# Performance work log

Measured on AMD Instinct MI355X. Metric: run time of the kernel, lower is better.

## Reference

```python
import jax, jax.numpy as jnp
import numpy as np

DIM = 1024
HEADS = 16
DIM_HEAD = 64
INNER = HEADS * DIM_HEAD
SCALE = 8.0  # default scale in plain_cosine_sim_attention
EPS = 1e-5


def setup_inputs() -> dict:
    key = jax.random.key(0)
    ks = jax.random.split(key, 5)
    b, n = 2, 2048
    x = jax.random.normal(ks[0], (b, n, DIM), dtype=jnp.float32)
    ln_w = jnp.ones((DIM,), dtype=jnp.float32)
    ln_b = jnp.zeros((DIM,), dtype=jnp.float32)
    W_qkv = jax.random.normal(ks[1], (DIM, 3 * INNER), dtype=jnp.float32) * (DIM ** -0.5)
    W_out = jax.random.normal(ks[2], (INNER, DIM), dtype=jnp.float32) * (INNER ** -0.5)
    return {"x": x, "ln_w": ln_w, "ln_b": ln_b, "W_qkv": W_qkv, "W_out": W_out}


def _l2norm(t):
    return t / jnp.clip(jnp.linalg.norm(t, axis=-1, keepdims=True), 1e-12)


def reference(x, ln_w, ln_b, W_qkv, W_out):
    b, n, _ = x.shape
    # LayerNorm
    mu = jnp.mean(x, axis=-1, keepdims=True)
    var = jnp.var(x, axis=-1, keepdims=True)
    xn = (x - mu) * jax.lax.rsqrt(var + EPS) * ln_w + ln_b
    # QKV projection (no bias)
    qkv = xn @ W_qkv  # [b, n, 3*inner]
    q, k, v = jnp.split(qkv, 3, axis=-1)
    # [b, n, h*d] -> [b, h, n, d]
    def to_heads(t):
        return t.reshape(b, n, HEADS, DIM_HEAD).transpose(0, 2, 1, 3)
    q, k, v = to_heads(q), to_heads(k), to_heads(v)
    # cosine-sim attention: l2-normalize q, k then scaled dot product
    q = _l2norm(q)
    k = _l2norm(k)
    sim = jnp.einsum('bhid,bhjd->bhij', q, k) * SCALE
    # causal mask
    causal = jnp.tril(jnp.ones((n, n), dtype=bool))
    sim = jnp.where(causal, sim, jnp.finfo(sim.dtype).min)
    attn = jax.nn.softmax(sim, axis=-1)
    o = jnp.einsum('bhij,bhjd->bhid', attn, v)
    # [b, h, n, d] -> [b, n, h*d]
    o = o.transpose(0, 2, 1, 3).reshape(b, n, INNER)
    return o @ W_out
```

## Files before the change

kernel.cpp:

```cpp
#include <hip/hip_runtime.h>
#include <hip/hip_bf16.h>

typedef __attribute__((ext_vector_type(8))) short short8;
typedef __attribute__((ext_vector_type(4))) float floatx4;

__device__ __forceinline__ ushort f2bf(float f) {
    union { __hip_bfloat16 h; ushort u; } cv;
    cv.h = __float2bfloat16(f);
    return cv.u;
}
__device__ __forceinline__ float bf2f(ushort u) {
    union { ushort u; __hip_bfloat16 h; } cv;
    cv.u = u;
    return __bfloat162float(cv.h);
}
__device__ __forceinline__ ushort f2bf_rtz(float f) {
    union { float f; unsigned u; } cv;
    cv.f = f;
    return (ushort)(cv.u >> 16);
}

typedef __attribute__((address_space(1))) void* gas1_t;
typedef __attribute__((address_space(3))) void* las3_t;
__device__ __forceinline__ void cp16(const ushort* g, ushort* l) {
    __builtin_amdgcn_global_load_lds((gas1_t)(unsigned long long)g,
                                     (las3_t)(unsigned long long)l, 16, 0, 0);
}

__global__ __launch_bounds__(256) void transpose_cast2(const float* __restrict__ Wqkv,
                                                       const float* __restrict__ Wout,
                                                       ushort* __restrict__ WqkvT,
                                                       ushort* __restrict__ WoutT) {
    __shared__ float tile[32][33];
    int bx = blockIdx.x, by = blockIdx.y;
    const float* in; ushort* out; int R = 1024, C;
    if (bx < 96) { in = Wqkv; out = WqkvT; C = 3072; }
    else { in = Wout; out = WoutT; C = 1024; bx -= 96; }
    int c0 = bx * 32, r0 = by * 32;
    int tx = threadIdx.x, ty = threadIdx.y;
    for (int j = 0; j < 32; j += 8)
        tile[ty + j][tx] = in[(size_t)(r0 + ty + j) * C + c0 + tx];
    __syncthreads();
    for (int j = 0; j < 32; j += 8)
        out[(size_t)(c0 + ty + j) * R + r0 + tx] = f2bf(tile[tx][ty + j]);
}

__global__ __launch_bounds__(256) void ln_kernel(const float* __restrict__ x,
                                                 const float* __restrict__ lw,
                                                 const float* __restrict__ lb,
                                                 ushort* __restrict__ xn) {
    int row = blockIdx.x;
    int tid = threadIdx.x;
    const float4* xr = (const float4*)(x + (size_t)row * 1024);
    float4 v = xr[tid];
    float s = v.x + v.y + v.z + v.w;
    float sq = v.x * v.x + v.y * v.y + v.z * v.z + v.w * v.w;
    for (int off = 32; off; off >>= 1) {
        s += __shfl_xor(s, off);
        sq += __shfl_xor(sq, off);
    }
    __shared__ float ls[4], lq[4];
    int wave = tid >> 6, lane = tid & 63;
    if (lane == 0) { ls[wave] = s; lq[wave] = sq; }
    __syncthreads();
    s = ls[0] + ls[1] + ls[2] + ls[3];
    sq = lq[0] + lq[1] + lq[2] + lq[3];
    float mu = s * (1.0f / 1024.0f);
    float var = sq * (1.0f / 1024.0f) - mu * mu;
    float rs = rsqrtf(var + 1e-5f);
    const float4* wr = (const float4*)lw;
    const float4* br = (const float4*)lb;
    float4 wv = wr[tid], bv = br[tid];
    ushort4 o;
    o.x = f2bf((v.x - mu) * rs * wv.x + bv.x);
    o.y = f2bf((v.y - mu) * rs * wv.y + bv.y);
    o.z = f2bf((v.z - mu) * rs * wv.z + bv.z);
    o.w = f2bf((v.w - mu) * rs * wv.w + bv.w);
    *(ushort4*)&xn[(size_t)row * 1024 + tid * 4] = o;
}

__global__ __launch_bounds__(256) void gemm_qkv_fused(const ushort* __restrict__ A,
                                                      const ushort* __restrict__ Bt,
                                                      ushort* __restrict__ Qt,
                                                      ushort* __restrict__ Kt,
                                                      ushort* __restrict__ Vb) {
    __shared__ ushort smem[18432];
    const int K = 1024, T = 32;
    const int tid = threadIdx.x;
    const int wave = tid >> 6, lane = tid & 63;
    const int quad = lane >> 4, l15 = lane & 15;
    const int wm = (wave >> 1) * 64, wn = (wave & 1) * 64;
    const int bm = blockIdx.y * 128, bn = blockIdx.x;

    const int s0 = tid, s1 = tid + 256;
    const int row0 = s0 >> 2, src0 = (s0 & 3) ^ (row0 & 3);
    const int row1 = s1 >> 2, src1 = (s1 & 3) ^ (row1 & 3);

    floatx4 acc[4][4];
    floatx4 z4 = {0.f, 0.f, 0.f, 0.f};
    for (int mi = 0; mi < 4; mi++)
        for (int ni = 0; ni < 4; ni++) acc[mi][ni] = z4;

    const ushort* Ap0 = A + (size_t)(bm + row0) * K + src0 * 8;
    const ushort* Ap1 = A + (size_t)(bm + row1) * K + src1 * 8;
    const ushort* Bp0 = Bt + (size_t)(bn * 128 + row0) * K + src0 * 8;
    const ushort* Bp1 = Bt + (size_t)(bn * 128 + row1) * K + src1 * 8;

    ushort* As = smem;
    ushort* Bs = smem + 8192;

    cp16(Ap0, &As[wave * 512]);
    cp16(Ap1, &As[2048 + wave * 512]);
    cp16(Bp0, &Bs[wave * 512]);
    cp16(Bp1, &Bs[2048 + wave * 512]);

    for (int t = 0; t < T; t++) {
        __syncthreads();
        if (t + 1 < T) {
            const int nb = (t + 1) & 1;
            const int k0n = (t + 1) << 5;
            cp16(Ap0 + k0n, &As[nb * 4096 + wave * 512]);
            cp16(Ap1 + k0n, &As[nb * 4096 + 2048 + wave * 512]);
            cp16(Bp0 + k0n, &Bs[nb * 4096 + wave * 512]);
            cp16(Bp1 + k0n, &Bs[nb * 4096 + 2048 + wave * 512]);
        }
        const ushort* Ab = As + (t & 1) * 4096;
        const ushort* Bb = Bs + (t & 1) * 4096;
        short8 af[4], bfr[4];
        for (int mi = 0; mi < 4; mi++) {
            int ra = wm + mi * 16 + l15;
            af[mi] = *(const short8*)&Ab[ra * 32 + ((quad ^ (ra & 3)) << 3)];
        }
        for (int ni = 0; ni < 4; ni++) {
            int rb = wn + ni * 16 + l15;
            bfr[ni] = *(const short8*)&Bb[rb * 32 + ((quad ^ (rb & 3)) << 3)];
        }
        for (int mi = 0; mi < 4; mi++)
            for (int ni = 0; ni < 4; ni++)
                acc[mi][ni] = __builtin_amdgcn_mfma_f32_16x16x32_bf16(
                    af[mi], bfr[ni], acc[mi][ni], 0, 0, 0);
    }

    const int col_base = bn * 128 + wn;
    const int type = col_base >> 10;
    const int h = (col_base & 1023) >> 6;
    const int row_base = bm + wm;

    if (type < 2) {
        ushort* dst = (type == 0) ? Qt : Kt;
        for (int mi = 0; mi < 4; mi++) {
            for (int r = 0; r < 4; r++) {
                float ss = 0.f;
                for (int ni = 0; ni < 4; ni++) ss += acc[mi][ni][r] * acc[mi][ni][r];
                for (int off = 1; off < 16; off <<= 1) ss += __shfl_xor(ss, off);
                float inv = rsqrtf(fmaxf(ss, 1e-24f));
                int rg = row_base + mi * 16 + quad * 4 + r;
                int bb = rg >> 11, n = rg & 2047;
                size_t orow = ((size_t)(bb * 16 + h) * 2048 + n) * 64;
                for (int ni = 0; ni < 4; ni++)
                    dst[orow + ni * 16 + l15] = f2bf(acc[mi][ni][r] * inv);
            }
        }
    } else {
        __syncthreads();
        ushort* tr = smem + wave * 4608;
        for (int mi = 0; mi < 4; mi++)
            for (int ni = 0; ni < 4; ni++)
                for (int r = 0; r < 4; r++) {
                    int row_l = mi * 16 + quad * 4 + r;
                    int col_l = ni * 16 + l15;
                    tr[col_l * 72 + row_l] = f2bf(acc[mi][ni][r]);
                }
        int bb = row_base >> 11, n0 = row_base & 2047;
        size_t vbase = ((size_t)(bb * 16 + h) * 32 + (n0 >> 6)) * 4096;
        const int dl = lane >> 3, nc = (lane & 7) * 8;
        for (int i = 0; i < 8; i++) {
            int d = dl + i * 8;
            short8 val = *(const short8*)&tr[d * 72 + nc];
            *(short8*)&Vb[vbase + (size_t)d * 64 + nc] = val;
        }
    }
}

__global__ __launch_bounds__(256) void gemm_out(const ushort* __restrict__ A,
                                                const ushort* __restrict__ Bt,
                                                float* __restrict__ C,
                                                int M, int N, int K) {
    __shared__ ushort As[2][128 * 32];
    __shared__ ushort Bs[2][128 * 32];
    const int tid = threadIdx.x;
    const int wave = tid >> 6, lane = tid & 63;
    const int quad = lane >> 4, l15 = lane & 15;
    const int wm = (wave >> 1) * 64, wn = (wave & 1) * 64;
    const int bm = blockIdx.y * 128, bn = blockIdx.x * 128;

    const int s0 = tid, s1 = tid + 256;
    const int row0 = s0 >> 2, src0 = (s0 & 3) ^ (row0 & 3);
    const int row1 = s1 >> 2, src1 = (s1 & 3) ^ (row1 & 3);

    floatx4 acc[4][4];
    floatx4 z4 = {0.f, 0.f, 0.f, 0.f};
    for (int mi = 0; mi < 4; mi++)
        for (int ni = 0; ni < 4; ni++) acc[mi][ni] = z4;

    const ushort* Ap0 = A + (size_t)(bm + row0) * K + src0 * 8;
    const ushort* Ap1 = A + (size_t)(bm + row1) * K + src1 * 8;
    const ushort* Bp0 = Bt + (size_t)(bn + row0) * K + src0 * 8;
    const ushort* Bp1 = Bt + (size_t)(bn + row1) * K + src1 * 8;

    const int T = K >> 5;
    cp16(Ap0, &As[0][wave * 512]);
    cp16(Ap1, &As[0][2048 + wave * 512]);
    cp16(Bp0, &Bs[0][wave * 512]);
    cp16(Bp1, &Bs[0][2048 + wave * 512]);

    for (int t = 0; t < T; t++) {
        __syncthreads();
        if (t + 1 < T) {
            const int nb = (t + 1) & 1;
            const int k0n = (t + 1) << 5;
            cp16(Ap0 + k0n, &As[nb][wave * 512]);
            cp16(Ap1 + k0n, &As[nb][2048 + wave * 512]);
            cp16(Bp0 + k0n, &Bs[nb][wave * 512]);
            cp16(Bp1 + k0n, &Bs[nb][2048 + wave * 512]);
        }
        const ushort* Ab = As[t & 1];
        const ushort* Bb = Bs[t & 1];
        short8 af[4], bfr[4];
        for (int mi = 0; mi < 4; mi++) {
            int ra = wm + mi * 16 + l15;
            af[mi] = *(const short8*)&Ab[ra * 32 + ((quad ^ (ra & 3)) << 3)];
        }
        for (int ni = 0; ni < 4; ni++) {
            int rb = wn + ni * 16 + l15;
            bfr[ni] = *(const short8*)&Bb[rb * 32 + ((quad ^ (rb & 3)) << 3)];
        }
        for (int mi = 0; mi < 4; mi++)
            for (int ni = 0; ni < 4; ni++)
                acc[mi][ni] = __builtin_amdgcn_mfma_f32_16x16x32_bf16(
                    af[mi], bfr[ni], acc[mi][ni], 0, 0, 0);
    }
    for (int mi = 0; mi < 4; mi++)
        for (int ni = 0; ni < 4; ni++)
            for (int r = 0; r < 4; r++) {
                int row = bm + wm + mi * 16 + quad * 4 + r;
                int col = bn + wn + ni * 16 + l15;
                C[(size_t)row * N + col] = acc[mi][ni][r];
            }
}

#define LOG2E8 11.541560327111707f

__global__ __launch_bounds__(256) void flash_attn(const ushort* __restrict__ Qt,
                                                  const ushort* __restrict__ Kt,
                                                  const ushort* __restrict__ Vb,
                                                  ushort* __restrict__ O) {
    const int id = blockIdx.x;
    const int xcd = id & 7, r_ = id >> 3;
    const int bh = xcd * 4 + (r_ >> 5);
    const int qt = r_ & 31;
    const int b = bh >> 4, h = bh & 15;
    const int q0 = qt * 64;
    const int tid = threadIdx.x;
    const int wave = tid >> 6, lane = tid & 63;
    const int quad = lane >> 4, l15 = lane & 15;

    __shared__ ushort Ks[2][64 * 64];
    __shared__ ushort Vs[2][64 * 64];
    __shared__ ushort Ps[4][16 * 64];

    const int ch0 = tid, ch1 = tid + 256;
    const int r0 = ch0 >> 3, sg0 = (ch0 & 7) ^ (r0 & 7);
    const int r1 = ch1 >> 3, sg1 = (ch1 & 7) ^ (r1 & 7);

    const ushort* Kp0 = Kt + ((size_t)bh * 2048 + r0) * 64 + sg0 * 8;
    const ushort* Kp1 = Kt + ((size_t)bh * 2048 + r1) * 64 + sg1 * 8;
    const ushort* Vp0 = Vb + (size_t)bh * 131072 + r0 * 64 + sg0 * 8;
    const ushort* Vp1 = Vb + (size_t)bh * 131072 + r1 * 64 + sg1 * 8;

    floatx4 z4 = {0.f, 0.f, 0.f, 0.f};

    const ushort* Qp = Qt + ((size_t)bh * 2048 + q0 + wave * 16 + l15) * 64;
    short8 qf0 = *(const short8*)(Qp + quad * 8);
    short8 qf1 = *(const short8*)(Qp + 32 + quad * 8);

    float rs_acc[4] = {0.f, 0.f, 0.f, 0.f};
    floatx4 o_acc[4];
    for (int ni = 0; ni < 4; ni++) o_acc[ni] = z4;

    cp16(Kp0, &Ks[0][wave * 512]);
    cp16(Kp1, &Ks[0][2048 + wave * 512]);
    cp16(Vp0, &Vs[0][wave * 512]);
    cp16(Vp1, &Vs[0][2048 + wave * 512]);

    for (int kt = 0; kt <= qt; kt++) {
        __syncthreads();
        if (kt < qt) {
            const int nb2 = (kt + 1) & 1;
            const size_t to = (size_t)(kt + 1) * 4096;
            cp16(Kp0 + to, &Ks[nb2][wave * 512]);
            cp16(Kp1 + to, &Ks[nb2][2048 + wave * 512]);
            cp16(Vp0 + to, &Vs[nb2][wave * 512]);
            cp16(Vp1 + to, &Vs[nb2][2048 + wave * 512]);
        }
        const ushort* Kb = Ks[kt & 1];
        const ushort* Vb_ = Vs[kt & 1];

        floatx4 s_acc[4];
        for (int ni = 0; ni < 4; ni++) s_acc[ni] = z4;
        for (int ni = 0; ni < 4; ni++) {
            int rb = ni * 16 + l15;
            short8 kf0 = *(const short8*)&Kb[rb * 64 + ((quad ^ (rb & 7)) << 3)];
            short8 kf1 = *(const short8*)&Kb[rb * 64 + (((quad + 4) ^ (rb & 7)) << 3)];
            s_acc[ni] = __builtin_amdgcn_mfma_f32_16x16x32_bf16(qf0, kf0, s_acc[ni], 0, 0, 0);
            s_acc[ni] = __builtin_amdgcn_mfma_f32_16x16x32_bf16(qf1, kf1, s_acc[ni], 0, 0, 0);
        }

        const bool diag = (kt == qt);
        for (int ni = 0; ni < 4; ni++) {
            const int col_loc = ni * 16 + l15;
            const int chnk = col_loc >> 3;
            for (int r = 0; r < 4; r++) {
                const int row_l = quad * 4 + r;
                float e = __builtin_amdgcn_exp2f(
                    fmaf(s_acc[ni][r], LOG2E8, -LOG2E8));
                if (diag && col_loc > wave * 16 + row_l) e = 0.f;
                rs_acc[r] += e;
                Ps[wave][row_l * 64 + (((chnk ^ (row_l & 7)) << 3) | (col_loc & 7))] =
                    f2bf_rtz(e);
            }
        }

        short8 pa0 = *(const short8*)&Ps[wave][l15 * 64 + ((quad ^ (l15 & 7)) << 3)];
        short8 pa1 = *(const short8*)&Ps[wave][l15 * 64 + (((quad + 4) ^ (l15 & 7)) << 3)];
        for (int ni = 0; ni < 4; ni++) {
            int rv = ni * 16 + l15;
            short8 v0 = *(const short8*)&Vb_[rv * 64 + ((quad ^ (rv & 7)) << 3)];
            short8 v1 = *(const short8*)&Vb_[rv * 64 + (((quad + 4) ^ (rv & 7)) << 3)];
            o_acc[ni] = __builtin_amdgcn_mfma_f32_16x16x32_bf16(pa0, v0, o_acc[ni], 0, 0, 0);
            o_acc[ni] = __builtin_amdgcn_mfma_f32_16x16x32_bf16(pa1, v1, o_acc[ni], 0, 0, 0);
        }
    }

    for (int r = 0; r < 4; r++) {
        float rs = rs_acc[r];
        for (int off = 1; off < 16; off <<= 1) rs += __shfl_xor(rs, off);
        float inv = 1.0f / rs;
        int grow = q0 + wave * 16 + quad * 4 + r;
        size_t rowbase = ((size_t)b * 2048 + grow) * 1024 + h * 64;
        for (int ni = 0; ni < 4; ni++)
            O[rowbase + ni * 16 + l15] = f2bf(o_acc[ni][r] * inv);
    }
}

extern "C" void kernel_launch(void* const* d_in, const int* in_sizes, int n_in,
                              void* d_out, int out_size, void* d_ws, size_t ws_size,
                              hipStream_t stream) {
    const float* x = (const float*)d_in[0];
    const float* ln_w = (const float*)d_in[1];
    const float* ln_b = (const float*)d_in[2];
    const float* W_qkv = (const float*)d_in[3];
    const float* W_out = (const float*)d_in[4];

    char* w = (char*)d_ws;
    ushort* xn    = (ushort*)(w);
    ushort* WqkvT = (ushort*)(w + (8ull << 20));
    ushort* WoutT = (ushort*)(w + (14ull << 20));
    ushort* Vb    = (ushort*)(w + (16ull << 20));
    ushort* Qt    = (ushort*)(w + (24ull << 20));
    ushort* Kt    = (ushort*)(w + (32ull << 20));
    ushort* obuf  = (ushort*)(w + (40ull << 20));

    transpose_cast2<<<dim3(128, 32), dim3(32, 8), 0, stream>>>(W_qkv, W_out, WqkvT, WoutT);
    ln_kernel<<<4096, 256, 0, stream>>>(x, ln_w, ln_b, xn);
    gemm_qkv_fused<<<dim3(24, 32), 256, 0, stream>>>(xn, WqkvT, Qt, Kt, Vb);
    flash_attn<<<1024, 256, 0, stream>>>(Qt, Kt, Vb, obuf);
    gemm_out<<<dim3(8, 32), 256, 0, stream>>>(obuf, WoutT, (float*)d_out, 4096, 1024, 1024);
}
```

Before: 191.2 us.

## Merge weight prep with layernorm, swizzle QKV GEMM grid, pair causal attention tiles

Three separate changes. The weight transpose/cast and layernorm now run as one launch, which removes a kernel boundary. The QKV GEMM grid becomes 1D with an XCD-aware remap, so blocks sharing A rows land on the same XCD for L2 reuse. Flash attention now has each block handle a pair of query tiles (i and 31-i), which balances causal work across blocks at the cost of halving the block count to 512 and serializing two passes.

Result: faster. 181.0 us (-5.3%).

```diff
diff --git a/kernel.cpp b/kernel.cpp
--- a/kernel.cpp
+++ b/kernel.cpp
@@ -27,56 +27,58 @@
                                      (las3_t)(unsigned long long)l, 16, 0, 0);
 }
 
-__global__ __launch_bounds__(256) void transpose_cast2(const float* __restrict__ Wqkv,
-                                                       const float* __restrict__ Wout,
-                                                       ushort* __restrict__ WqkvT,
-                                                       ushort* __restrict__ WoutT) {
-    __shared__ float tile[32][33];
-    int bx = blockIdx.x, by = blockIdx.y;
-    const float* in; ushort* out; int R = 1024, C;
-    if (bx < 96) { in = Wqkv; out = WqkvT; C = 3072; }
-    else { in = Wout; out = WoutT; C = 1024; bx -= 96; }
-    int c0 = bx * 32, r0 = by * 32;
-    int tx = threadIdx.x, ty = threadIdx.y;
-    for (int j = 0; j < 32; j += 8)
-        tile[ty + j][tx] = in[(size_t)(r0 + ty + j) * C + c0 + tx];
-    __syncthreads();
-    for (int j = 0; j < 32; j += 8)
-        out[(size_t)(c0 + ty + j) * R + r0 + tx] = f2bf(tile[tx][ty + j]);
-}
-
-__global__ __launch_bounds__(256) void ln_kernel(const float* __restrict__ x,
+__global__ __launch_bounds__(256) void prep_w_ln(const float* __restrict__ Wqkv,
+                                                 const float* __restrict__ Wout,
+                                                 ushort* __restrict__ WqkvT,
+                                                 ushort* __restrict__ WoutT,
+                                                 const float* __restrict__ x,
                                                  const float* __restrict__ lw,
                                                  const float* __restrict__ lb,
                                                  ushort* __restrict__ xn) {
-    int row = blockIdx.x;
-    int tid = threadIdx.x;
-    const float4* xr = (const float4*)(x + (size_t)row * 1024);
-    float4 v = xr[tid];
-    float s = v.x + v.y + v.z + v.w;
-    float sq = v.x * v.x + v.y * v.y + v.z * v.z + v.w * v.w;
-    for (int off = 32; off; off >>= 1) {
-        s += __shfl_xor(s, off);
-        sq += __shfl_xor(sq, off);
-    }
-    __shared__ float ls[4], lq[4];
-    int wave = tid >> 6, lane = tid & 63;
-    if (lane == 0) { ls[wave] = s; lq[wave] = sq; }
-    __syncthreads();
-    s = ls[0] + ls[1] + ls[2] + ls[3];
-    sq = lq[0] + lq[1] + lq[2] + lq[3];
-    float mu = s * (1.0f / 1024.0f);
-    float var = sq * (1.0f / 1024.0f) - mu * mu;
-    float rs = rsqrtf(var + 1e-5f);
-    const float4* wr = (const float4*)lw;
-    const float4* br = (const float4*)lb;
-    float4 wv = wr[tid], bv = br[tid];
-    ushort4 o;
-    o.x = f2bf((v.x - mu) * rs * wv.x + bv.x);
-    o.y = f2bf((v.y - mu) * rs * wv.y + bv.y);
-    o.z = f2bf((v.z - mu) * rs * wv.z + bv.z);
-    o.w = f2bf((v.w - mu) * rs * wv.w + bv.w);
-    *(ushort4*)&xn[(size_t)row * 1024 + tid * 4] = o;
+    const int id = blockIdx.x;
+    const int tid = threadIdx.x;
+    if (id < 4096) {
+        __shared__ float tile[32][33];
+        int bx = id & 127, by = id >> 7;
+        const float* in; ushort* out; int R = 1024, C;
+        if (bx < 96) { in = Wqkv; out = WqkvT; C = 3072; }
+        else { in = Wout; out = WoutT; C = 1024; bx -= 96; }
+        int c0 = bx * 32, r0 = by * 32;
+        int tx = tid & 31, ty = tid >> 5;
+        for (int j = 0; j < 32; j += 8)
+            tile[ty + j][tx] = in[(size_t)(r0 + ty + j) * C + c0 + tx];
+        __syncthreads();
+        for (int j = 0; j < 32; j += 8)
+            out[(size_t)(c0 + ty + j) * R + r0 + tx] = f2bf(tile[tx][ty + j]);
+    } else {
+        int row = id - 4096;
+        const float4* xr = (const float4*)(x + (size_t)row * 1024);
+        float4 v = xr[tid];
+        float s = v.x + v.y + v.z + v.w;
+        float sq = v.x * v.x + v.y * v.y + v.z * v.z + v.w * v.w;
+        for (int off = 32; off; off >>= 1) {
+            s += __shfl_xor(s, off);
+            sq += __shfl_xor(sq, off);
+        }
+        __shared__ float ls[4], lq[4];
+        int wave = tid >> 6, lane = tid & 63;
+        if (lane == 0) { ls[wave] = s; lq[wave] = sq; }
+        __syncthreads();
+        s = ls[0] + ls[1] + ls[2] + ls[3];
+        sq = lq[0] + lq[1] + lq[2] + lq[3];
+        float mu = s * (1.0f / 1024.0f);
+        float var = sq * (1.0f / 1024.0f) - mu * mu;
+        float rs = rsqrtf(var + 1e-5f);
+        const float4* wr = (const float4*)lw;
+        const float4* br = (const float4*)lb;
+        float4 wv = wr[tid], bv = br[tid];
+        ushort4 o;
+        o.x = f2bf((v.x - mu) * rs * wv.x + bv.x);
+        o.y = f2bf((v.y - mu) * rs * wv.y + bv.y);
+        o.z = f2bf((v.z - mu) * rs * wv.z + bv.z);
+        o.w = f2bf((v.w - mu) * rs * wv.w + bv.w);
+        *(ushort4*)&xn[(size_t)row * 1024 + tid * 4] = o;
+    }
 }
 
 __global__ __launch_bounds__(256) void gemm_qkv_fused(const ushort* __restrict__ A,
@@ -86,11 +88,14 @@
                                                       ushort* __restrict__ Vb) {
     __shared__ ushort smem[18432];
     const int K = 1024, T = 32;
+    const int id = blockIdx.x;
+    const int xcd = id & 7, r_ = id >> 3;
+    const int bm = (xcd * 4 + r_ / 24) * 128;
+    const int bn = r_ % 24;
     const int tid = threadIdx.x;
     const int wave = tid >> 6, lane = tid & 63;
     const int quad = lane >> 4, l15 = lane & 15;
     const int wm = (wave >> 1) * 64, wn = (wave & 1) * 64;
-    const int bm = blockIdx.y * 128, bn = blockIdx.x;
 
     const int s0 = tid, s1 = tid + 256;
     const int row0 = s0 >> 2, src0 = (s0 & 3) ^ (row0 & 3);
@@ -257,10 +262,9 @@
                                                   ushort* __restrict__ O) {
     const int id = blockIdx.x;
     const int xcd = id & 7, r_ = id >> 3;
-    const int bh = xcd * 4 + (r_ >> 5);
-    const int qt = r_ & 31;
+    const int bh = xcd * 4 + (r_ >> 4);
+    const int pairi = r_ & 15;
     const int b = bh >> 4, h = bh & 15;
-    const int q0 = qt * 64;
     const int tid = threadIdx.x;
     const int wave = tid >> 6, lane = tid & 63;
     const int quad = lane >> 4, l15 = lane & 15;
@@ -280,76 +284,82 @@
 
     floatx4 z4 = {0.f, 0.f, 0.f, 0.f};
 
-    const ushort* Qp = Qt + ((size_t)bh * 2048 + q0 + wave * 16 + l15) * 64;
-    short8 qf0 = *(const short8*)(Qp + quad * 8);
-    short8 qf1 = *(const short8*)(Qp + 32 + quad * 8);
-
-    float rs_acc[4] = {0.f, 0.f, 0.f, 0.f};
-    floatx4 o_acc[4];
-    for (int ni = 0; ni < 4; ni++) o_acc[ni] = z4;
-
-    cp16(Kp0, &Ks[0][wave * 512]);
-    cp16(Kp1, &Ks[0][2048 + wave * 512]);
-    cp16(Vp0, &Vs[0][wave * 512]);
-    cp16(Vp1, &Vs[0][2048 + wave * 512]);
-
-    for (int kt = 0; kt <= qt; kt++) {
-        __syncthreads();
-        if (kt < qt) {
-            const int nb2 = (kt + 1) & 1;
-            const size_t to = (size_t)(kt + 1) * 4096;
-            cp16(Kp0 + to, &Ks[nb2][wave * 512]);
-            cp16(Kp1 + to, &Ks[nb2][2048 + wave * 512]);
-            cp16(Vp0 + to, &Vs[nb2][wave * 512]);
-            cp16(Vp1 + to, &Vs[nb2][2048 + wave * 512]);
-        }
-        const ushort* Kb = Ks[kt & 1];
-        const ushort* Vb_ = Vs[kt & 1];
-
-        floatx4 s_acc[4];
-        for (int ni = 0; ni < 4; ni++) s_acc[ni] = z4;
-        for (int ni = 0; ni < 4; ni++) {
-            int rb = ni * 16 + l15;
-            short8 kf0 = *(const short8*)&Kb[rb * 64 + ((quad ^ (rb & 7)) << 3)];
-            short8 kf1 = *(const short8*)&Kb[rb * 64 + (((quad + 4) ^ (rb & 7)) << 3)];
-            s_acc[ni] = __builtin_amdgcn_mfma_f32_16x16x32_bf16(qf0, kf0, s_acc[ni], 0, 0, 0);
-            s_acc[ni] = __builtin_amdgcn_mfma_f32_16x16x32_bf16(qf1, kf1, s_acc[ni], 0, 0, 0);
-        }
-
-        const bool diag = (kt == qt);
-        for (int ni = 0; ni < 4; ni++) {
-            const int col_loc = ni * 16 + l15;
-            const int chnk = col_loc >> 3;
-            for (int r = 0; r < 4; r++) {
-                const int row_l = quad * 4 + r;
-                float e = __builtin_amdgcn_exp2f(
-                    fmaf(s_acc[ni][r], LOG2E8, -LOG2E8));
-                if (diag && col_loc > wave * 16 + row_l) e = 0.f;
-                rs_acc[r] += e;
-                Ps[wave][row_l * 64 + (((chnk ^ (row_l & 7)) << 3) | (col_loc & 7))] =
-                    f2bf_rtz(e);
-            }
-        }
-
-        short8 pa0 = *(const short8*)&Ps[wave][l15 * 64 + ((quad ^ (l15 & 7)) << 3)];
-        short8 pa1 = *(const short8*)&Ps[wave][l15 * 64 + (((quad + 4) ^ (l15 & 7)) << 3)];
-        for (int ni = 0; ni < 4; ni++) {
-            int rv = ni * 16 + l15;
-            short8 v0 = *(const short8*)&Vb_[rv * 64 + ((quad ^ (rv & 7)) << 3)];
-            short8 v1 = *(const short8*)&Vb_[rv * 64 + (((quad + 4) ^ (rv & 7)) << 3)];
-            o_acc[ni] = __builtin_amdgcn_mfma_f32_16x16x32_bf16(pa0, v0, o_acc[ni], 0, 0, 0);
-            o_acc[ni] = __builtin_amdgcn_mfma_f32_16x16x32_bf16(pa1, v1, o_acc[ni], 0, 0, 0);
-        }
-    }
-
-    for (int r = 0; r < 4; r++) {
-        float rs = rs_acc[r];
-        for (int off = 1; off < 16; off <<= 1) rs += __shfl_xor(rs, off);
-        float inv = 1.0f / rs;
-        int grow = q0 + wave * 16 + quad * 4 + r;
-        size_t rowbase = ((size_t)b * 2048 + grow) * 1024 + h * 64;
-        for (int ni = 0; ni < 4; ni++)
-            O[rowbase + ni * 16 + l15] = f2bf(o_acc[ni][r] * inv);
+    for (int pass = 0; pass < 2; pass++) {
+        const int qt = pass ? (31 - pairi) : pairi;
+        const int q0 = qt * 64;
+
+        const ushort* Qp = Qt + ((size_t)bh * 2048 + q0 + wave * 16 + l15) * 64;
+        short8 qf0 = *(const short8*)(Qp + quad * 8);
+        short8 qf1 = *(const short8*)(Qp + 32 + quad * 8);
+
+        float rs_acc[4] = {0.f, 0.f, 0.f, 0.f};
+        floatx4 o_acc[4];
+        for (int ni = 0; ni < 4; ni++) o_acc[ni] = z4;
+
+        __syncthreads();
+        cp16(Kp0, &Ks[0][wave * 512]);
+        cp16(Kp1, &Ks[0][2048 + wave * 512]);
+        cp16(Vp0, &Vs[0][wave * 512]);
+        cp16(Vp1, &Vs[0][2048 + wave * 512]);
+
+        for (int kt = 0; kt <= qt; kt++) {
+            __syncthreads();
+            if (kt < qt) {
+                const int nb2 = (kt + 1) & 1;
+                const size_t to = (size_t)(kt + 1) * 4096;
+                cp16(Kp0 + to, &Ks[nb2][wave * 512]);
+                cp16(Kp1 + to, &Ks[nb2][2048 + wave * 512]);
+                cp16(Vp0 + to, &Vs[nb2][wave * 512]);
+                cp16(Vp1 + to, &Vs[nb2][2048 + wave * 512]);
+            }
+            const ushort* Kb = Ks[kt & 1];
+            const ushort* Vb_ = Vs[kt & 1];
+
+            floatx4 s_acc[4];
+            for (int ni = 0; ni < 4; ni++) s_acc[ni] = z4;
+            for (int ni = 0; ni < 4; ni++) {
+                int rb = ni * 16 + l15;
+                short8 kf0 = *(const short8*)&Kb[rb * 64 + ((quad ^ (rb & 7)) << 3)];
+                short8 kf1 = *(const short8*)&Kb[rb * 64 + (((quad + 4) ^ (rb & 7)) << 3)];
+                s_acc[ni] = __builtin_amdgcn_mfma_f32_16x16x32_bf16(qf0, kf0, s_acc[ni], 0, 0, 0);
+                s_acc[ni] = __builtin_amdgcn_mfma_f32_16x16x32_bf16(qf1, kf1, s_acc[ni], 0, 0, 0);
+            }
+
+            const bool diag = (kt == qt);
+            for (int ni = 0; ni < 4; ni++) {
+                const int col_loc = ni * 16 + l15;
+                const int chnk = col_loc >> 3;
+                for (int r = 0; r < 4; r++) {
+                    const int row_l = quad * 4 + r;
+                    float e = __builtin_amdgcn_exp2f(
+                        fmaf(s_acc[ni][r], LOG2E8, -LOG2E8));
+                    if (diag && col_loc > wave * 16 + row_l) e = 0.f;
+                    rs_acc[r] += e;
+                    Ps[wave][row_l * 64 + (((chnk ^ (row_l & 7)) << 3) | (col_loc & 7))] =
+                        f2bf_rtz(e);
+                }
+            }
+
+            short8 pa0 = *(const short8*)&Ps[wave][l15 * 64 + ((quad ^ (l15 & 7)) << 3)];
+            short8 pa1 = *(const short8*)&Ps[wave][l15 * 64 + (((quad + 4) ^ (l15 & 7)) << 3)];
+            for (int ni = 0; ni < 4; ni++) {
+                int rv = ni * 16 + l15;
+                short8 v0 = *(const short8*)&Vb_[rv * 64 + ((quad ^ (rv & 7)) << 3)];
+                short8 v1 = *(const short8*)&Vb_[rv * 64 + (((quad + 4) ^ (rv & 7)) << 3)];
+                o_acc[ni] = __builtin_amdgcn_mfma_f32_16x16x32_bf16(pa0, v0, o_acc[ni], 0, 0, 0);
+                o_acc[ni] = __builtin_amdgcn_mfma_f32_16x16x32_bf16(pa1, v1, o_acc[ni], 0, 0, 0);
+            }
+        }
+
+        for (int r = 0; r < 4; r++) {
+            float rs = rs_acc[r];
+            for (int off = 1; off < 16; off <<= 1) rs += __shfl_xor(rs, off);
+            float inv = 1.0f / rs;
+            int grow = q0 + wave * 16 + quad * 4 + r;
+            size_t rowbase = ((size_t)b * 2048 + grow) * 1024 + h * 64;
+            for (int ni = 0; ni < 4; ni++)
+                O[rowbase + ni * 16 + l15] = f2bf(o_acc[ni][r] * inv);
+        }
     }
 }
 
@@ -371,9 +381,8 @@
     ushort* Kt    = (ushort*)(w + (32ull << 20));
     ushort* obuf  = (ushort*)(w + (40ull << 20));
 
-    transpose_cast2<<<dim3(128, 32), dim3(32, 8), 0, stream>>>(W_qkv, W_out, WqkvT, WoutT);
-    ln_kernel<<<4096, 256, 0, stream>>>(x, ln_w, ln_b, xn);
-    gemm_qkv_fused<<<dim3(24, 32), 256, 0, stream>>>(xn, WqkvT, Qt, Kt, Vb);
-    flash_attn<<<1024, 256, 0, stream>>>(Qt, Kt, Vb, obuf);
+    prep_w_ln<<<8192, 256, 0, stream>>>(W_qkv, W_out, WqkvT, WoutT, x, ln_w, ln_b, xn);
+    gemm_qkv_fused<<<768, 256, 0, stream>>>(xn, WqkvT, Qt, Kt, Vb);
+    flash_attn<<<512, 256, 0, stream>>>(Qt, Kt, Vb, obuf);
     gemm_out<<<dim3(8, 32), 256, 0, stream>>>(obuf, WoutT, (float*)d_out, 4096, 1024, 1024);
 }
```
